# Kernel tuning notes

Measured on AMD Instinct MI355X. Metric: run time of the kernel, lower is better.

## Reference

```python
import jax, jax.numpy as jnp
import numpy as np

DROPOUT_P = 0.2
HEAD_SIZE = 64
EMBED = 1024


def setup_inputs() -> dict:
    key = jax.random.key(0)
    kx, kk, kq, kv = jax.random.split(key, 4)
    B, T = 4, 4096
    x = jax.random.normal(kx, (B, T, EMBED), dtype=jnp.float32)
    # torch Linear(embed, head, bias=False): y = x @ W.T with W [head, embed].
    # We store W_* as [embed, head] so projection is x @ W.
    scale = 1.0 / np.sqrt(EMBED)
    Wk = jax.random.uniform(kk, (EMBED, HEAD_SIZE), jnp.float32, -scale, scale)
    Wq = jax.random.uniform(kq, (EMBED, HEAD_SIZE), jnp.float32, -scale, scale)
    Wv = jax.random.uniform(kv, (EMBED, HEAD_SIZE), jnp.float32, -scale, scale)
    return {"x": x, "Wk": Wk, "Wq": Wq, "Wv": Wv}


def reference(x, Wk, Wq, Wv):
    # Projections: [B,T,E] @ [E,H] -> [B,T,H]
    k = jnp.einsum("bte,eh->bth", x, Wk)
    q = jnp.einsum("bte,eh->bth", x, Wq)
    v = jnp.einsum("bte,eh->bth", x, Wv)
    # Raw scaled scores, NO softmax: [B,T,T]
    w = jnp.einsum("bqh,bkh->bqk", q, k) * (HEAD_SIZE ** -0.5)
    # Dropout (training mode, inverted scaling) with a fixed key.
    keep = jax.random.bernoulli(jax.random.key(42), 1.0 - DROPOUT_P, w.shape)
    w = jnp.where(keep, w / (1.0 - DROPOUT_P), 0.0)
    # Weighted V sum: [B,T,T] @ [B,T,H] -> [B,T,H]
    return jnp.einsum("bqk,bkh->bqh", w, v)
```

## Files before the change

kernel.cpp:

```cpp
#include <hip/hip_runtime.h>


#define TB 4
#define TT 4096
#define TE 1024
#define TH 64
#define COMB_SCALE 0.15625f

typedef __bf16 bf16x8 __attribute__((ext_vector_type(8)));
typedef __bf16 bf16x4 __attribute__((ext_vector_type(4)));
typedef float  f32x4  __attribute__((ext_vector_type(4)));

#define ROTL(x, d) __builtin_amdgcn_alignbit((x), (x), 32u - (d))

__device__ __forceinline__ unsigned tf_bits(unsigned j) {
  const unsigned ks1 = 42u;
  const unsigned ks2 = 0x1BD11BDAu ^ 42u;
  unsigned x0 = 0u, x1 = j + ks1;
#define TF_RND(d) { x0 += x1; x1 = ROTL(x1, (d)); x1 ^= x0; }
  TF_RND(13u) TF_RND(15u) TF_RND(26u) TF_RND(6u)
  x0 += ks1; x1 += ks2 + 1u;
  TF_RND(17u) TF_RND(29u) TF_RND(16u) TF_RND(24u)
  x0 += ks2; x1 += 0u + 2u;
  TF_RND(13u) TF_RND(15u) TF_RND(26u) TF_RND(6u)
  x0 += 0u;  x1 += ks1 + 3u;
  TF_RND(17u) TF_RND(29u) TF_RND(16u) TF_RND(24u)
  x0 += ks1; x1 += ks2 + 4u;
  TF_RND(13u) TF_RND(15u) TF_RND(26u) TF_RND(6u)
  x0 += ks2; x1 += 0u + 5u;
#undef TF_RND
  return x0 ^ x1;
}

__device__ __forceinline__ unsigned tf_keepmask(unsigned j) {
  return tf_bits(j) < 3435974144u ? 0xFFFFFFFFu : 0u;
}

__global__ __launch_bounds__(256)
void prep_wt(const float* __restrict__ Wq, const float* __restrict__ Wk,
             const float* __restrict__ Wv, __bf16* __restrict__ WT)
{
  __shared__ float lds[64][65];
  const int wi = blockIdx.x >> 4;
  const int k0 = (blockIdx.x & 15) * 64;
  const float* W = (wi == 0) ? Wq : ((wi == 1) ? Wk : Wv);
  const int tid = threadIdx.x;
#pragma unroll
  for (int it = 0; it < 16; ++it) {
    const int idx = tid + it * 256;
    lds[idx >> 6][idx & 63] = W[(size_t)(k0 + (idx >> 6)) * TH + (idx & 63)];
  }
  __syncthreads();
#pragma unroll
  for (int it = 0; it < 16; ++it) {
    const int idx = tid + it * 256;
    const int n = idx >> 6, kk = idx & 63;
    WT[(size_t)(wi * TH + n) * TE + k0 + kk] = (__bf16)lds[kk][n];
  }
}

__global__ __launch_bounds__(256, 3)
void proj_mfma(const float* __restrict__ x, const __bf16* __restrict__ WT,
               __bf16* __restrict__ qs, __bf16* __restrict__ ks,
               __bf16* __restrict__ vT)
{
  __shared__ float red[4][16][196];
  const int tid = threadIdx.x;
  const int w  = tid >> 6, l = tid & 63;
  const int l4 = l >> 4,  lm = l & 15;
  const int R  = blockIdx.x * 16;

  const float*  xr = x  + (size_t)(R + lm) * TE + w * 256;
  const __bf16* wt = WT + (size_t)lm * TE + w * 256;

  f32x4 acc[12];
#pragma unroll
  for (int t = 0; t < 12; ++t) acc[t] = (f32x4){0.f, 0.f, 0.f, 0.f};

#pragma unroll
  for (int k0 = 0; k0 < 256; k0 += 32) {
    const float4 u0 = *reinterpret_cast<const float4*>(xr + k0 + l4 * 8);
    const float4 u1 = *reinterpret_cast<const float4*>(xr + k0 + l4 * 8 + 4);
    bf16x8 am;
    am[0] = (__bf16)u0.x; am[1] = (__bf16)u0.y;
    am[2] = (__bf16)u0.z; am[3] = (__bf16)u0.w;
    am[4] = (__bf16)u1.x; am[5] = (__bf16)u1.y;
    am[6] = (__bf16)u1.z; am[7] = (__bf16)u1.w;
    bf16x8 bn[12];
#pragma unroll
    for (int t = 0; t < 12; ++t)
      bn[t] = *reinterpret_cast<const bf16x8*>(wt + (size_t)t * 16 * TE + k0 + l4 * 8);
#pragma unroll
    for (int t = 0; t < 12; ++t)
      acc[t] = __builtin_amdgcn_mfma_f32_16x16x32_bf16(am, bn[t], acc[t], 0, 0, 0);
  }

#pragma unroll
  for (int t = 0; t < 12; ++t)
#pragma unroll
    for (int r = 0; r < 4; ++r)
      red[w][l4 * 4 + r][t * 16 + lm] = acc[t][r];
  __syncthreads();

  const int row0 = R + l4 * 4;
#pragma unroll
  for (int t2 = 0; t2 < 3; ++t2) {
    const int n = w * 48 + t2 * 16 + lm;
    float v[4];
#pragma unroll
    for (int r = 0; r < 4; ++r) {
      const int rr = l4 * 4 + r;
      v[r] = red[0][rr][n] + red[1][rr][n] + red[2][rr][n] + red[3][rr][n];
    }
    if (n < TH) {
#pragma unroll
      for (int r = 0; r < 4; ++r)
        qs[(size_t)(row0 + r) * TH + n] = (__bf16)(v[r] * COMB_SCALE);
    } else if (n < 2 * TH) {
#pragma unroll
      for (int r = 0; r < 4; ++r)
        ks[(size_t)(row0 + r) * TH + (n - TH)] = (__bf16)v[r];
    } else {
      bf16x4 vv;
#pragma unroll
      for (int r = 0; r < 4; ++r) vv[r] = (__bf16)v[r];
      const int bb = row0 >> 12, trow = row0 & (TT - 1);
      *reinterpret_cast<bf16x4*>(
          vT + ((size_t)(bb * TH + (n - 2 * TH)) * TT + trow)) = vv;
    }
  }
}

__global__ __launch_bounds__(256, 4)
void attn_mfma(const __bf16* __restrict__ qs,
               const __bf16* __restrict__ ks,
               const __bf16* __restrict__ vT,
               float* __restrict__ out)
{
  __shared__ __bf16 S_lds[4][16 * 64];
  __shared__ float  Oex[3][16][TH + 4];

  const int tid = threadIdx.x;
  const int w   = tid >> 6;
  const int l   = tid & 63;
  const int l4  = l >> 4;
  const int lm  = l & 15;

  const int b     = blockIdx.x >> 8;
  const int qt16  = blockIdx.x & 255;
  const int qrow0 = qt16 * 16;
  const int kv0   = w * (TT / 4);

  const __bf16* qb = qs + ((size_t)b * TT + qrow0) * TH;
  const bf16x8 qf0 = *reinterpret_cast<const bf16x8*>(qb + (size_t)lm * TH + l4 * 8);
  const bf16x8 qf1 = *reinterpret_cast<const bf16x8*>(qb + (size_t)lm * TH + 32 + l4 * 8);

  const __bf16* kbp = ks + (size_t)b * TT * TH;
  const __bf16* vbp = vT + (size_t)b * TH * TT;

  f32x4 o_acc[4];
#pragma unroll
  for (int t = 0; t < 4; ++t) o_acc[t] = (f32x4){0.f, 0.f, 0.f, 0.f};

  const unsigned base0 = ((unsigned)(b * TT) + (unsigned)qrow0 + (unsigned)(l4 * 4)) * (unsigned)TT;
  const unsigned sw = (unsigned)((lm & 7) << 3);

  for (int kb = kv0; kb < kv0 + TT / 4; kb += 64) {
    bf16x8 kf[4][2];
#pragma unroll
    for (int t = 0; t < 4; ++t) {
      const __bf16* kr = kbp + (size_t)(kb + t * 16 + lm) * TH;
#pragma unroll
      for (int ss = 0; ss < 2; ++ss)
        kf[t][ss] = *reinterpret_cast<const bf16x8*>(kr + ss * 32 + l4 * 8);
    }
    bf16x8 vf[4][2];
#pragma unroll
    for (int t = 0; t < 4; ++t) {
      const __bf16* vr = vbp + (size_t)(t * 16 + lm) * TT + kb;
#pragma unroll
      for (int ss = 0; ss < 2; ++ss)
        vf[t][ss] = *reinterpret_cast<const bf16x8*>(vr + ss * 32 + l4 * 8);
    }

    unsigned km[4][4];
    const unsigned jcol = (unsigned)kb + (unsigned)lm;
#pragma unroll
    for (int t = 0; t < 4; ++t)
#pragma unroll
      for (int r = 0; r < 4; ++r)
        km[t][r] = tf_keepmask(base0 + (unsigned)(r << 12) + jcol + (unsigned)(t << 4));

    __builtin_amdgcn_s_setprio(1);
    f32x4 sa[4];
#pragma unroll
    for (int t = 0; t < 4; ++t) {
      f32x4 c = {0.f, 0.f, 0.f, 0.f};
      c = __builtin_amdgcn_mfma_f32_16x16x32_bf16(qf0, kf[t][0], c, 0, 0, 0);
      c = __builtin_amdgcn_mfma_f32_16x16x32_bf16(qf1, kf[t][1], c, 0, 0, 0);
      sa[t] = c;
    }
    __builtin_amdgcn_s_setprio(0);

#pragma unroll
    for (int t = 0; t < 4; ++t) {
#pragma unroll
      for (int r = 0; r < 4; ++r) {
        const unsigned sb = __float_as_uint(sa[t][r]) & km[t][r];
        const int row = l4 * 4 + r;
        const int col = t * 16 + lm;
        S_lds[w][row * 64 + (col ^ ((row & 7) << 3))] =
            (__bf16)__uint_as_float(sb);
      }
    }

    const bf16x8 af0 = *reinterpret_cast<const bf16x8*>(
        &S_lds[w][lm * 64 + ((unsigned)(l4 * 8) ^ sw)]);
    const bf16x8 af1 = *reinterpret_cast<const bf16x8*>(
        &S_lds[w][lm * 64 + ((unsigned)(32 + l4 * 8) ^ sw)]);

    __builtin_amdgcn_s_setprio(1);
#pragma unroll
    for (int t = 0; t < 4; ++t) {
      o_acc[t] = __builtin_amdgcn_mfma_f32_16x16x32_bf16(af0, vf[t][0], o_acc[t], 0, 0, 0);
      o_acc[t] = __builtin_amdgcn_mfma_f32_16x16x32_bf16(af1, vf[t][1], o_acc[t], 0, 0, 0);
    }
    __builtin_amdgcn_s_setprio(0);
  }

  if (w > 0) {
#pragma unroll
    for (int t = 0; t < 4; ++t)
#pragma unroll
      for (int r = 0; r < 4; ++r)
        Oex[w - 1][l4 * 4 + r][t * 16 + lm] = o_acc[t][r];
  }
  __syncthreads();
  if (w == 0) {
    float* outb = out + ((size_t)b * TT + qrow0) * TH;
#pragma unroll
    for (int t = 0; t < 4; ++t)
#pragma unroll
      for (int r = 0; r < 4; ++r) {
        const int row = l4 * 4 + r, col = t * 16 + lm;
        outb[(size_t)row * TH + col] = o_acc[t][r] + Oex[0][row][col] +
                                       Oex[1][row][col] + Oex[2][row][col];
      }
  }
}

extern "C" void kernel_launch(void* const* d_in, const int* in_sizes, int n_in,
                              void* d_out, int out_size, void* d_ws, size_t ws_size,
                              hipStream_t stream) {
  const float* x  = (const float*)d_in[0];
  const float* Wk = (const float*)d_in[1];
  const float* Wq = (const float*)d_in[2];
  const float* Wv = (const float*)d_in[3];
  float* outp = (float*)d_out;

  const size_t SZ = (size_t)TB * TT * TH;
  __bf16* q_ws  = (__bf16*)d_ws;
  __bf16* k_ws  = q_ws + SZ;
  __bf16* vT_ws = k_ws + SZ;
  __bf16* WT_ws = vT_ws + SZ;

  prep_wt<<<dim3(48), dim3(256), 0, stream>>>(Wq, Wk, Wv, WT_ws);
  proj_mfma<<<dim3(TB * TT / 16), dim3(256), 0, stream>>>(
      x, WT_ws, q_ws, k_ws, vT_ws);
  attn_mfma<<<dim3(TB * (TT / 16)), dim3(256), 0, stream>>>(
      q_ws, k_ws, vT_ws, outp);
}
```

Before: 191.5 us.

## Split attention KV range across two blocks and add combine kernel

Doubles the attention grid so each block handles half of the key/value sequence, writing fp32 partial outputs to workspace, then a separate kernel sums the two partials. LDS for the score staging and cross-wave reduction buffers is aliased to cut shared memory per block. The intent is more parallelism and better tail balance, at the cost of extra global traffic for partials and an additional kernel launch.

```diff
diff --git a/kernel.cpp b/kernel.cpp
--- a/kernel.cpp
+++ b/kernel.cpp
@@ -135,10 +135,11 @@
 void attn_mfma(const __bf16* __restrict__ qs,
                const __bf16* __restrict__ ks,
                const __bf16* __restrict__ vT,
-               float* __restrict__ out)
-{
-  __shared__ __bf16 S_lds[4][16 * 64];
-  __shared__ float  Oex[3][16][TH + 4];
+               float* __restrict__ Opart)
+{
+  __shared__ __align__(16) char smem[13312];
+  __bf16 (*S_lds)[16 * 64] = reinterpret_cast<__bf16(*)[16 * 64]>(smem);
+  float (*Oex)[16][TH + 4]  = reinterpret_cast<float(*)[16][TH + 4]>(smem);
 
   const int tid = threadIdx.x;
   const int w   = tid >> 6;
@@ -146,10 +147,12 @@
   const int l4  = l >> 4;
   const int lm  = l & 15;
 
-  const int b     = blockIdx.x >> 8;
-  const int qt16  = blockIdx.x & 255;
+  const int kvh   = blockIdx.x >> 10;
+  const int A     = blockIdx.x & 1023;
+  const int b     = A >> 8;
+  const int qt16  = A & 255;
   const int qrow0 = qt16 * 16;
-  const int kv0   = w * (TT / 4);
+  const int kv0   = kvh * (TT / 2) + w * (TT / 8);
 
   const __bf16* qb = qs + ((size_t)b * TT + qrow0) * TH;
   const bf16x8 qf0 = *reinterpret_cast<const bf16x8*>(qb + (size_t)lm * TH + l4 * 8);
@@ -165,7 +168,7 @@
   const unsigned base0 = ((unsigned)(b * TT) + (unsigned)qrow0 + (unsigned)(l4 * 4)) * (unsigned)TT;
   const unsigned sw = (unsigned)((lm & 7) << 3);
 
-  for (int kb = kv0; kb < kv0 + TT / 4; kb += 64) {
+  for (int kb = kv0; kb < kv0 + TT / 8; kb += 64) {
     bf16x8 kf[4][2];
 #pragma unroll
     for (int t = 0; t < 4; ++t) {
@@ -228,6 +231,7 @@
     __builtin_amdgcn_s_setprio(0);
   }
 
+  __syncthreads();
   if (w > 0) {
 #pragma unroll
     for (int t = 0; t < 4; ++t)
@@ -237,7 +241,8 @@
   }
   __syncthreads();
   if (w == 0) {
-    float* outb = out + ((size_t)b * TT + qrow0) * TH;
+    float* outb = Opart + (size_t)kvh * ((size_t)TB * TT * TH) +
+                  ((size_t)b * TT + qrow0) * TH;
 #pragma unroll
     for (int t = 0; t < 4; ++t)
 #pragma unroll
@@ -247,6 +252,17 @@
                                        Oex[1][row][col] + Oex[2][row][col];
       }
   }
+}
+
+__global__ __launch_bounds__(256)
+void combine(const float* __restrict__ Opart, float* __restrict__ out)
+{
+  const size_t i = ((size_t)blockIdx.x * 256 + threadIdx.x) * 4;
+  const float4 a = *reinterpret_cast<const float4*>(Opart + i);
+  const float4 c = *reinterpret_cast<const float4*>(Opart + (size_t)TB * TT * TH + i);
+  float4 s;
+  s.x = a.x + c.x; s.y = a.y + c.y; s.z = a.z + c.z; s.w = a.w + c.w;
+  *reinterpret_cast<float4*>(out + i) = s;
 }
 
 extern "C" void kernel_launch(void* const* d_in, const int* in_sizes, int n_in,
@@ -263,10 +279,12 @@
   __bf16* k_ws  = q_ws + SZ;
   __bf16* vT_ws = k_ws + SZ;
   __bf16* WT_ws = vT_ws + SZ;
+  float*  Opart = (float*)(WT_ws + 192 * TE);
 
   prep_wt<<<dim3(48), dim3(256), 0, stream>>>(Wq, Wk, Wv, WT_ws);
   proj_mfma<<<dim3(TB * TT / 16), dim3(256), 0, stream>>>(
       x, WT_ws, q_ws, k_ws, vT_ws);
-  attn_mfma<<<dim3(TB * (TT / 16)), dim3(256), 0, stream>>>(
-      q_ws, k_ws, vT_ws, outp);
-}
+  attn_mfma<<<dim3(TB * (TT / 16) * 2), dim3(256), 0, stream>>>(
+      q_ws, k_ws, vT_ws, Opart);
+  combine<<<dim3(SZ / 4 / 256), dim3(256), 0, stream>>>(Opart, outp);
+}
```

Result: no change. 193.7 us (+1.1%).
